# Kernel optimization log

Hardware: AMD Instinct MI355X
Metric: run time of the kernel (lower is better)

Reference implementation:

```python
import jax, jax.numpy as jnp
import numpy as np

D_MODEL = 1024
N_HEADS = 16
D_HEAD = D_MODEL // N_HEADS
D_FF = 4096
B, T = 2, 2048


def layer_norm(x, gamma, beta, eps=1e-5):
    mu = jnp.mean(x, axis=-1, keepdims=True)
    var = jnp.var(x, axis=-1, keepdims=True)
    return (x - mu) * jax.lax.rsqrt(var + eps) * gamma + beta


def setup_inputs() -> dict:
    key = jax.random.key(0)
    ks = jax.random.split(key, 8)
    s = D_MODEL ** -0.5
    return {
        "x": jax.random.normal(ks[0], (B, T, D_MODEL), dtype=jnp.float32),
        "w_qkv": jax.random.normal(ks[1], (D_MODEL, 3 * D_MODEL), dtype=jnp.float32) * s,
        "w_out": jax.random.normal(ks[2], (D_MODEL, D_MODEL), dtype=jnp.float32) * s,
        "ln1_g": jnp.ones((D_MODEL,), jnp.float32),
        "ln1_b": jnp.zeros((D_MODEL,), jnp.float32),
        "ln2_g": jnp.ones((D_MODEL,), jnp.float32),
        "ln2_b": jnp.zeros((D_MODEL,), jnp.float32),
        "w1": jax.random.normal(ks[3], (D_MODEL, D_FF), dtype=jnp.float32) * s,
        "b1": jnp.zeros((D_FF,), jnp.float32),
        "w2": jax.random.normal(ks[4], (D_FF, D_MODEL), dtype=jnp.float32) * (D_FF ** -0.5),
        "b2": jnp.zeros((D_MODEL,), jnp.float32),
    }


def reference(x, w_qkv, w_out, ln1_g, ln1_b, ln2_g, ln2_b, w1, b1, w2, b2):
    Bb, Tt, C = x.shape
    h = layer_norm(x, ln1_g, ln1_b)
    qkv = h @ w_qkv  # [B,T,3C]
    q, k, v = jnp.split(qkv, 3, axis=-1)

    def heads(t):  # [B,T,C] -> [B,H,T,Dh]
        return t.reshape(Bb, Tt, N_HEADS, D_HEAD).transpose(0, 2, 1, 3)

    q, k, v = heads(q), heads(k), heads(v)
    scale = D_HEAD ** -0.5
    attn = jnp.einsum("bhqd,bhkd->bhqk", q, k) * scale
    causal = jnp.tril(jnp.ones((Tt, Tt), dtype=bool))
    attn = jnp.where(causal[None, None], attn, -jnp.inf)
    attn = jax.nn.softmax(attn, axis=-1)
    out = jnp.einsum("bhqk,bhkd->bhqd", attn, v)
    out = out.transpose(0, 2, 1, 3).reshape(Bb, Tt, C)
    x = x + out @ w_out
    h2 = layer_norm(x, ln2_g, ln2_b)
    ff = jax.nn.gelu(h2 @ w1 + b1, approximate=False) @ w2 + b2
    return x + ff
```

## Files before the change

kernel.cpp:

```cpp
#include <hip/hip_runtime.h>
#include <hip/hip_bf16.h>
#include <cstdint>

#define DM 1024
#define DFF 4096
#define NB 2
#define TT 2048
#define NH 16
#define DH 64

typedef unsigned short u16;
typedef __bf16 bf16x8 __attribute__((ext_vector_type(8)));
typedef float f32x4 __attribute__((ext_vector_type(4)));

__device__ __forceinline__ u16 f2b(float f) {
    union { float f; unsigned u; } v; v.f = f;
    unsigned u = v.u;
    return (u16)((u + 0x7FFFu + ((u >> 16) & 1u)) >> 16);
}

__device__ __forceinline__ unsigned cvtpk(float a, float b) {
    unsigned r;
    asm("v_cvt_pk_bf16_f32 %0, %1, %2" : "=v"(r) : "v"(a), "v"(b));
    return r;
}

__device__ __forceinline__ float gelu_fast(float z) {
    const float u = z * z;
    const float w = z * __builtin_fmaf(u, 0.10294324f, 2.3022082f);
    const float e = exp2f(w);
    const float r = __builtin_amdgcn_rcpf(1.0f + e);
    return z - z * r;
}

__device__ __forceinline__ f32x4 mfma_bf16(bf16x8 a, bf16x8 b, f32x4 c) {
    return __builtin_amdgcn_mfma_f32_16x16x32_bf16(a, b, c, 0, 0, 0);
}

__device__ __forceinline__ void gload_lds16(const void* g, void* l) {
    __builtin_amdgcn_global_load_lds((const __attribute__((address_space(1))) unsigned int*)g,
                                     (__attribute__((address_space(3))) unsigned int*)l, 16, 0, 0);
}

__global__ __launch_bounds__(256) void transW(const float* __restrict__ W, u16* __restrict__ Wt,
                                              int K, int N) {
    __shared__ float t[32][33];
    int tx = threadIdx.x & 31, ty = threadIdx.x >> 5;
    int k0 = blockIdx.y * 32, n0 = blockIdx.x * 32;
#pragma unroll
    for (int j = 0; j < 4; ++j)
        t[ty + 8 * j][tx] = W[(size_t)(k0 + ty + 8 * j) * N + n0 + tx];
    __syncthreads();
#pragma unroll
    for (int j = 0; j < 4; ++j)
        Wt[(size_t)(n0 + ty + 8 * j) * K + k0 + tx] = f2b(t[tx][ty + 8 * j]);
}

__global__ __launch_bounds__(256) void ln_kernel(const float* __restrict__ X,
                                                 const float* __restrict__ g,
                                                 const float* __restrict__ bt,
                                                 u16* __restrict__ H) {
    int row = blockIdx.x, tid = threadIdx.x;
    float4 v = ((const float4*)(X + (size_t)row * DM))[tid];
    float s = v.x + v.y + v.z + v.w;
    float ss = v.x * v.x + v.y * v.y + v.z * v.z + v.w * v.w;
#pragma unroll
    for (int off = 32; off >= 1; off >>= 1) {
        s += __shfl_xor(s, off);
        ss += __shfl_xor(ss, off);
    }
    __shared__ float sb[8];
    int w = tid >> 6, lane = tid & 63;
    if (lane == 0) { sb[w] = s; sb[4 + w] = ss; }
    __syncthreads();
    s = sb[0] + sb[1] + sb[2] + sb[3];
    ss = sb[4] + sb[5] + sb[6] + sb[7];
    float mu = s * (1.0f / DM);
    float var = ss * (1.0f / DM) - mu * mu;
    float rstd = rsqrtf(var + 1e-5f);
    float4 gv = ((const float4*)g)[tid];
    float4 bv = ((const float4*)bt)[tid];
    uint2 hv;
    hv.x = cvtpk((v.x - mu) * rstd * gv.x + bv.x, (v.y - mu) * rstd * gv.y + bv.y);
    hv.y = cvtpk((v.z - mu) * rstd * gv.z + bv.z, (v.w - mu) * rstd * gv.w + bv.w);
    ((uint2*)(H + (size_t)row * DM))[tid] = hv;
}

template <int MODE, int DBUF>
__global__ __launch_bounds__(256) void gemm_kernel(
    const u16* __restrict__ A, const u16* __restrict__ Bt, int M, int N, int K,
    u16* __restrict__ oq, u16* __restrict__ ok, u16* __restrict__ vt,
    const float* __restrict__ resid, float* __restrict__ outf,
    const float* __restrict__ bias, u16* __restrict__ outbf) {
    __shared__ __align__(16) u16 Alds[DBUF + 1][128][64];
    __shared__ __align__(16) u16 Blds[DBUF + 1][128][64];
    const int tid = threadIdx.x;
    const int lane = tid & 63;
    const int w = tid >> 6;
    const int wr = w >> 1, wc = w & 1;
    int bid = blockIdx.x + gridDim.x * blockIdx.y;
    const int nwg = gridDim.x * gridDim.y;
    bid = (bid & 7) * (nwg >> 3) + (bid >> 3);
    const int bm = (bid / gridDim.x) * 128, bn = (bid % gridDim.x) * 128;
    const int l15 = lane & 15, lg = lane >> 4;
    const int srow = tid >> 3, pch = tid & 7;
    const int lc = pch ^ (srow & 7);

    f32x4 acc[4][4] = {};
    const u16* Ap = A + (size_t)(bm + srow) * K + lc * 8;
    const u16* Bp = Bt + (size_t)(bn + srow) * K + lc * 8;

#define STAGE(buf, k0)                                                          \
    {                                                                           \
        _Pragma("unroll") for (int i = 0; i < 4; ++i) {                         \
            gload_lds16(Ap + (size_t)(32 * i) * K + (k0), &Alds[buf][srow + 32 * i][pch * 8]); \
            gload_lds16(Bp + (size_t)(32 * i) * K + (k0), &Blds[buf][srow + 32 * i][pch * 8]); \
        }                                                                       \
    }

#define COMPUTE(buf)                                                            \
    {                                                                           \
        _Pragma("unroll") for (int kk = 0; kk < 2; ++kk) {                      \
            bf16x8 af[4], bfr[4];                                               \
            _Pragma("unroll") for (int f = 0; f < 4; ++f) {                     \
                const int ar = wr * 64 + f * 16 + l15;                          \
                const int br = wc * 64 + f * 16 + l15;                          \
                const int kch = kk * 4 + lg;                                    \
                af[f] = *(const bf16x8*)&Alds[buf][ar][(kch ^ (ar & 7)) * 8];   \
                bfr[f] = *(const bf16x8*)&Blds[buf][br][(kch ^ (br & 7)) * 8];  \
            }                                                                   \
            _Pragma("unroll") for (int mi = 0; mi < 4; ++mi)                    \
                _Pragma("unroll") for (int ni = 0; ni < 4; ++ni)                \
                    acc[mi][ni] = mfma_bf16(af[mi], bfr[ni], acc[mi][ni]);      \
        }                                                                       \
    }

    if constexpr (DBUF == 0) {
        for (int k0 = 0; k0 < K; k0 += 64) {
            STAGE(0, k0);
            __syncthreads();
            COMPUTE(0);
            __syncthreads();
        }
    } else {
        STAGE(0, 0);
        for (int k0 = 0; k0 < K; k0 += 64) {
            const int cur = (k0 >> 6) & 1;
            if (k0 + 64 < K) {
                STAGE(cur ^ 1, k0 + 64);
                asm volatile("s_waitcnt vmcnt(8)" ::: "memory");
            } else {
                asm volatile("s_waitcnt vmcnt(0)" ::: "memory");
            }
            __builtin_amdgcn_sched_barrier(0);
            __builtin_amdgcn_s_barrier();
            __builtin_amdgcn_sched_barrier(0);
            COMPUTE(cur);
            __builtin_amdgcn_s_barrier();
        }
    }
#undef STAGE
#undef COMPUTE

    const int m0 = bm + wr * 64, n0 = bn + wc * 64;
#pragma unroll
    for (int mi = 0; mi < 4; ++mi) {
#pragma unroll
        for (int ni = 0; ni < 4; ++ni) {
            if constexpr (MODE == 0) {
                const int n = n0 + ni * 16 + l15;
                const int which = n >> 10;
                const int hh = (n >> 6) & 15, d = n & 63;
                const int mbase = m0 + mi * 16 + 4 * lg;
                const int bb = mbase >> 11, t = mbase & 2047;
                if (which == 2) {
                    uint2 pv;
                    pv.x = cvtpk(acc[mi][ni][0], acc[mi][ni][1]);
                    pv.y = cvtpk(acc[mi][ni][2], acc[mi][ni][3]);
                    *(uint2*)(vt + (((size_t)(bb * NH + hh)) * DH + d) * TT + t) = pv;
                } else {
                    u16* dst = which == 0 ? oq : ok;
                    const float sc = which == 0 ? 0.18033688f : 1.0f;
                    const unsigned p01 = cvtpk(acc[mi][ni][0] * sc, acc[mi][ni][1] * sc);
                    const unsigned p23 = cvtpk(acc[mi][ni][2] * sc, acc[mi][ni][3] * sc);
                    u16* db = dst + (((size_t)(bb * NH + hh)) * TT + t) * DH + d;
                    db[0] = (u16)p01;
                    db[DH] = (u16)(p01 >> 16);
                    db[2 * DH] = (u16)p23;
                    db[3 * DH] = (u16)(p23 >> 16);
                }
            } else if constexpr (MODE == 2) {
                const int n = n0 + ni * 16 + l15;
                const float bn_ = bias[n];
                const float g0 = gelu_fast(acc[mi][ni][0] + bn_);
                const float g1 = gelu_fast(acc[mi][ni][1] + bn_);
                const float g2 = gelu_fast(acc[mi][ni][2] + bn_);
                const float g3 = gelu_fast(acc[mi][ni][3] + bn_);
                const unsigned p01 = cvtpk(g0, g1);
                const unsigned p23 = cvtpk(g2, g3);
                u16* db = outbf + (size_t)(m0 + mi * 16 + 4 * lg) * N + n;
                db[0] = (u16)p01;
                db[N] = (u16)(p01 >> 16);
                db[2 * N] = (u16)p23;
                db[3 * N] = (u16)(p23 >> 16);
            } else {
#pragma unroll
                for (int r = 0; r < 4; ++r) {
                    int m = m0 + mi * 16 + 4 * lg + r;
                    int n = n0 + ni * 16 + l15;
                    float v = acc[mi][ni][r];
                    size_t o = (size_t)m * N + n;
                    if constexpr (MODE == 1) {
                        outf[o] = resid[o] + v;
                    } else {
                        outf[o] = resid[o] + v + bias[n];
                    }
                }
            }
        }
    }
}

__global__ __launch_bounds__(256) void attn_kernel(const u16* __restrict__ Q,
                                                   const u16* __restrict__ Kg,
                                                   const u16* __restrict__ Vtg,
                                                   u16* __restrict__ O) {
    __shared__ __align__(16) u16 Klds[2][64][64];
    __shared__ __align__(16) u16 Vlds[2][64][64];
    const int tid = threadIdx.x, lane = tid & 63, w = tid >> 6;
    const int l15 = lane & 15, lg = lane >> 4;

    int id = blockIdx.x + (blockIdx.y << 4);
    int sw = (id & 7) * 64 + (id >> 3);
    const int p = sw & 15, bh = sw >> 4;
    const size_t base = (size_t)bh * TT * DH;
    const int b = bh >> 4, hh = bh & 15;

    const int srow = tid >> 3, pch = tid & 7;
    const int lc = pch ^ (srow & 7);

    const int src0 = (((2 * lg) & 3) << 4) | l15;
    const int src1 = src0 + 16;
    const bool hi = (lg >> 1) != 0;

#define ASTAGE(buf, kv)                                                                     \
    {                                                                                       \
        gload_lds16(Kg + base + (size_t)((kv) * 64 + srow) * DH + lc * 8,                   \
                    &Klds[buf][srow][pch * 8]);                                             \
        gload_lds16(Kg + base + (size_t)((kv) * 64 + srow + 32) * DH + lc * 8,              \
                    &Klds[buf][srow + 32][pch * 8]);                                        \
        gload_lds16(Vtg + base + (size_t)srow * TT + (kv) * 64 + lc * 8,                    \
                    &Vlds[buf][srow][pch * 8]);                                             \
        gload_lds16(Vtg + base + (size_t)(srow + 32) * TT + (kv) * 64 + lc * 8,             \
                    &Vlds[buf][srow + 32][pch * 8]);                                        \
    }

    for (int half = 0; half < 2; ++half) {
        const int qt = half ? (31 - p) : p;
        const int nkv = qt + 1;
        const int qrow = qt * 64 + w * 16 + l15;
        uint4 qu0 = *(const uint4*)(Q + base + (size_t)qrow * DH + 8 * lg);
        uint4 qu1 = *(const uint4*)(Q + base + (size_t)qrow * DH + 32 + 8 * lg);
        asm volatile("" : "+v"(qu0.x), "+v"(qu0.y), "+v"(qu0.z), "+v"(qu0.w),
                          "+v"(qu1.x), "+v"(qu1.y), "+v"(qu1.z), "+v"(qu1.w));
        const bf16x8 qf0 = *(const bf16x8*)&qu0;
        const bf16x8 qf1 = *(const bf16x8*)&qu1;

        ASTAGE(0, 0);

        f32x4 o[4] = {};
        float mrun = -INFINITY, lsum = 0.0f;

        int cur = 0;
        for (int kv = 0; kv < nkv; ++kv) {
            if (kv + 1 < nkv) {
                ASTAGE(cur ^ 1, kv + 1);
                asm volatile("s_waitcnt vmcnt(4)" ::: "memory");
            } else {
                asm volatile("s_waitcnt vmcnt(0)" ::: "memory");
            }
            __builtin_amdgcn_sched_barrier(0);
            __builtin_amdgcn_s_barrier();
            __builtin_amdgcn_sched_barrier(0);

            f32x4 s[4] = {};
            __builtin_amdgcn_s_setprio(1);
#pragma unroll
            for (int nf = 0; nf < 4; ++nf) {
                const int row = nf * 16 + l15;
                bf16x8 kb0 = *(const bf16x8*)&Klds[cur][row][(lg ^ (l15 & 7)) * 8];
                bf16x8 kb1 = *(const bf16x8*)&Klds[cur][row][((4 + lg) ^ (l15 & 7)) * 8];
                s[nf] = mfma_bf16(kb0, qf0, s[nf]);
                s[nf] = mfma_bf16(kb1, qf1, s[nf]);
            }
            __builtin_amdgcn_s_setprio(0);

            if (kv == qt) {
#pragma unroll
                for (int nf = 0; nf < 4; ++nf) {
                    const int tg = kv * 64 + nf * 16 + 4 * lg;
#pragma unroll
                    for (int r = 0; r < 4; ++r)
                        if (tg + r > qrow) s[nf][r] = -1e30f;
                }
            }

            f32x4 m4 = s[0];
#pragma unroll
            for (int nf = 1; nf < 4; ++nf) {
                m4[0] = fmaxf(m4[0], s[nf][0]);
                m4[1] = fmaxf(m4[1], s[nf][1]);
                m4[2] = fmaxf(m4[2], s[nf][2]);
                m4[3] = fmaxf(m4[3], s[nf][3]);
            }
            float pmax = fmaxf(fmaxf(m4[0], m4[1]), fmaxf(m4[2], m4[3]));
            pmax = fmaxf(pmax, __shfl_xor(pmax, 16));
            pmax = fmaxf(pmax, __shfl_xor(pmax, 32));
            const float mnew = fmaxf(mrun, pmax);
            const float alpha = exp2f(mrun - mnew);
            mrun = mnew;
            float ps = 0.0f;
#pragma unroll
            for (int nf = 0; nf < 4; ++nf) {
#pragma unroll
                for (int r = 0; r < 4; ++r) {
                    const float pp = exp2f(s[nf][r] - mnew);
                    s[nf][r] = pp;
                    ps += pp;
                }
                o[nf] = o[nf] * alpha;
            }
            lsum = lsum * alpha + ps;

            unsigned pk[4][2];
#pragma unroll
            for (int nf = 0; nf < 4; ++nf) {
                pk[nf][0] = cvtpk(s[nf][0], s[nf][1]);
                pk[nf][1] = cvtpk(s[nf][2], s[nf][3]);
            }
            bf16x8 pa[2];
#pragma unroll
            for (int kf = 0; kf < 2; ++kf) {
                unsigned a0 = __shfl((int)pk[2 * kf][0], src0);
                unsigned a1 = __shfl((int)pk[2 * kf][1], src0);
                unsigned a2 = __shfl((int)pk[2 * kf][0], src1);
                unsigned a3 = __shfl((int)pk[2 * kf][1], src1);
                unsigned c0 = __shfl((int)pk[2 * kf + 1][0], src0);
                unsigned c1 = __shfl((int)pk[2 * kf + 1][1], src0);
                unsigned c2 = __shfl((int)pk[2 * kf + 1][0], src1);
                unsigned c3 = __shfl((int)pk[2 * kf + 1][1], src1);
                uint4 wv;
                wv.x = hi ? c0 : a0;
                wv.y = hi ? c1 : a1;
                wv.z = hi ? c2 : a2;
                wv.w = hi ? c3 : a3;
                pa[kf] = *(const bf16x8*)&wv;
            }

            __builtin_amdgcn_s_setprio(1);
#pragma unroll
            for (int nf = 0; nf < 4; ++nf) {
                const int row = nf * 16 + l15;
                bf16x8 vb0 = *(const bf16x8*)&Vlds[cur][row][(lg ^ (l15 & 7)) * 8];
                bf16x8 vb1 = *(const bf16x8*)&Vlds[cur][row][((4 + lg) ^ (l15 & 7)) * 8];
                o[nf] = mfma_bf16(vb0, pa[0], o[nf]);
                o[nf] = mfma_bf16(vb1, pa[1], o[nf]);
            }
            __builtin_amdgcn_s_setprio(0);

            __builtin_amdgcn_s_barrier();
            cur ^= 1;
        }

        lsum += __shfl_xor(lsum, 16);
        lsum += __shfl_xor(lsum, 32);
        const float linv = 1.0f / lsum;
#pragma unroll
        for (int nf = 0; nf < 4; ++nf) {
            uint2 pv;
            pv.x = cvtpk(o[nf][0] * linv, o[nf][1] * linv);
            pv.y = cvtpk(o[nf][2] * linv, o[nf][3] * linv);
            *(uint2*)(O + ((size_t)b * TT + qrow) * DM + hh * DH + nf * 16 + 4 * lg) = pv;
        }
    }
#undef ASTAGE
}

extern "C" void kernel_launch(void* const* d_in, const int* in_sizes, int n_in,
                              void* d_out, int out_size, void* d_ws, size_t ws_size,
                              hipStream_t stream) {
    const float* x = (const float*)d_in[0];
    const float* wqkv = (const float*)d_in[1];
    const float* wout = (const float*)d_in[2];
    const float* ln1g = (const float*)d_in[3];
    const float* ln1b = (const float*)d_in[4];
    const float* ln2g = (const float*)d_in[5];
    const float* ln2b = (const float*)d_in[6];
    const float* w1 = (const float*)d_in[7];
    const float* b1 = (const float*)d_in[8];
    const float* w2 = (const float*)d_in[9];
    const float* b2 = (const float*)d_in[10];
    float* out = (float*)d_out;
    char* ws = (char*)d_ws;

    u16* wqkv_t = (u16*)(ws + 0);
    u16* wout_t = (u16*)(ws + 6291456);
    u16* w1_t   = (u16*)(ws + 8388608);
    u16* w2_t   = (u16*)(ws + 16777216);
    u16* h_bf   = (u16*)(ws + 25165824);
    u16* q_bf   = (u16*)(ws + 33554432);
    u16* k_bf   = (u16*)(ws + 41943040);
    u16* vt_bf  = (u16*)(ws + 50331648);
    u16* at_bf  = (u16*)(ws + 58720256);
    float* x1   = (float*)(ws + 67108864);
    u16* ff1_bf = q_bf;

    transW<<<dim3(96, 32), 256, 0, stream>>>(wqkv, wqkv_t, 1024, 3072);
    transW<<<dim3(32, 32), 256, 0, stream>>>(wout, wout_t, 1024, 1024);
    transW<<<dim3(128, 32), 256, 0, stream>>>(w1, w1_t, 1024, 4096);
    transW<<<dim3(32, 128), 256, 0, stream>>>(w2, w2_t, 4096, 1024);

    ln_kernel<<<4096, 256, 0, stream>>>(x, ln1g, ln1b, h_bf);

    gemm_kernel<0, 1><<<dim3(24, 32), 256, 0, stream>>>(h_bf, wqkv_t, 4096, 3072, 1024,
                                                        q_bf, k_bf, vt_bf,
                                                        nullptr, nullptr, nullptr, nullptr);

    attn_kernel<<<dim3(16, 32), 256, 0, stream>>>(q_bf, k_bf, vt_bf, at_bf);

    gemm_kernel<1, 1><<<dim3(8, 32), 256, 0, stream>>>(at_bf, wout_t, 4096, 1024, 1024,
                                                       nullptr, nullptr, nullptr,
                                                       x, x1, nullptr, nullptr);

    ln_kernel<<<4096, 256, 0, stream>>>(x1, ln2g, ln2b, h_bf);

    gemm_kernel<2, 1><<<dim3(32, 32), 256, 0, stream>>>(h_bf, w1_t, 4096, 4096, 1024,
                                                        nullptr, nullptr, nullptr,
                                                        nullptr, nullptr, b1, ff1_bf);

    gemm_kernel<3, 1><<<dim3(8, 32), 256, 0, stream>>>(ff1_bf, w2_t, 4096, 1024, 4096,
                                                       nullptr, nullptr, nullptr,
                                                       x1, out, b2, nullptr);
}
```

Before: 262.7 us.

## Split-K the FFN down-projection GEMM and add lazy softmax rescaling in attention

The final w2 GEMM (K=4096) now launches twice as many workgroups, each covering half of K. The second half writes raw partial sums into a workspace buffer that a new elementwise add kernel folds into the output. This targets low occupancy: the original grid had only 256 tiles for a long K loop. Attention also skips the running-max update and the rescale of the accumulator and sum unless some lane's new max exceeds the old one by more than 8 (in log2 units). That trades a wavefront vote for fewer multiplies, at the cost of an extra launch and 32MB of extra memory traffic for the partial buffer.

```diff
diff --git a/kernel.cpp b/kernel.cpp
--- a/kernel.cpp
+++ b/kernel.cpp
@@ -86,12 +86,25 @@
     ((uint2*)(H + (size_t)row * DM))[tid] = hv;
 }
 
-template <int MODE, int DBUF>
+__global__ __launch_bounds__(256) void add_kernel(float* __restrict__ out,
+                                                  const float* __restrict__ part, int n4) {
+    int idx = blockIdx.x * 256 + threadIdx.x;
+    const int stride = gridDim.x * 256;
+    for (; idx < n4; idx += stride) {
+        float4 a = ((const float4*)out)[idx];
+        float4 p = ((const float4*)part)[idx];
+        a.x += p.x; a.y += p.y; a.z += p.z; a.w += p.w;
+        ((float4*)out)[idx] = a;
+    }
+}
+
+template <int MODE, int DBUF, int SPLIT>
 __global__ __launch_bounds__(256) void gemm_kernel(
     const u16* __restrict__ A, const u16* __restrict__ Bt, int M, int N, int K,
     u16* __restrict__ oq, u16* __restrict__ ok, u16* __restrict__ vt,
     const float* __restrict__ resid, float* __restrict__ outf,
-    const float* __restrict__ bias, u16* __restrict__ outbf) {
+    const float* __restrict__ bias, u16* __restrict__ outbf,
+    float* __restrict__ part) {
     __shared__ __align__(16) u16 Alds[DBUF + 1][128][64];
     __shared__ __align__(16) u16 Blds[DBUF + 1][128][64];
     const int tid = threadIdx.x;
@@ -101,7 +114,16 @@
     int bid = blockIdx.x + gridDim.x * blockIdx.y;
     const int nwg = gridDim.x * gridDim.y;
     bid = (bid & 7) * (nwg >> 3) + (bid >> 3);
-    const int bm = (bid / gridDim.x) * 128, bn = (bid % gridDim.x) * 128;
+    int mrow = bid / gridDim.x;
+    int ks = 0;
+    if constexpr (SPLIT) {
+        const int mtiles = (nwg / gridDim.x) >> 1;
+        ks = mrow >= mtiles;
+        mrow -= ks * mtiles;
+    }
+    const int bm = mrow * 128, bn = (bid % gridDim.x) * 128;
+    const int kbeg = SPLIT ? ks * (K >> 1) : 0;
+    const int kend = SPLIT ? kbeg + (K >> 1) : K;
     const int l15 = lane & 15, lg = lane >> 4;
     const int srow = tid >> 3, pch = tid & 7;
     const int lc = pch ^ (srow & 7);
@@ -136,17 +158,17 @@
     }
 
     if constexpr (DBUF == 0) {
-        for (int k0 = 0; k0 < K; k0 += 64) {
+        for (int k0 = kbeg; k0 < kend; k0 += 64) {
             STAGE(0, k0);
             __syncthreads();
             COMPUTE(0);
             __syncthreads();
         }
     } else {
-        STAGE(0, 0);
-        for (int k0 = 0; k0 < K; k0 += 64) {
-            const int cur = (k0 >> 6) & 1;
-            if (k0 + 64 < K) {
+        STAGE(0, kbeg);
+        for (int k0 = kbeg; k0 < kend; k0 += 64) {
+            const int cur = ((k0 - kbeg) >> 6) & 1;
+            if (k0 + 64 < kend) {
                 STAGE(cur ^ 1, k0 + 64);
                 asm volatile("s_waitcnt vmcnt(8)" ::: "memory");
             } else {
@@ -213,7 +235,10 @@
                     if constexpr (MODE == 1) {
                         outf[o] = resid[o] + v;
                     } else {
-                        outf[o] = resid[o] + v + bias[n];
+                        if (SPLIT && ks == 1)
+                            part[o] = v;
+                        else
+                            outf[o] = resid[o] + v + bias[n];
                     }
                 }
             }
@@ -316,21 +341,25 @@
             float pmax = fmaxf(fmaxf(m4[0], m4[1]), fmaxf(m4[2], m4[3]));
             pmax = fmaxf(pmax, __shfl_xor(pmax, 16));
             pmax = fmaxf(pmax, __shfl_xor(pmax, 32));
-            const float mnew = fmaxf(mrun, pmax);
-            const float alpha = exp2f(mrun - mnew);
-            mrun = mnew;
+            if (!__all(pmax <= mrun + 8.0f)) {
+                const float mnew = fmaxf(mrun, pmax);
+                const float alpha = exp2f(mrun - mnew);
+                mrun = mnew;
+#pragma unroll
+                for (int nf = 0; nf < 4; ++nf) o[nf] = o[nf] * alpha;
+                lsum *= alpha;
+            }
             float ps = 0.0f;
 #pragma unroll
             for (int nf = 0; nf < 4; ++nf) {
 #pragma unroll
                 for (int r = 0; r < 4; ++r) {
-                    const float pp = exp2f(s[nf][r] - mnew);
+                    const float pp = exp2f(s[nf][r] - mrun);
                     s[nf][r] = pp;
                     ps += pp;
                 }
-                o[nf] = o[nf] * alpha;
-            }
-            lsum = lsum * alpha + ps;
+            }
+            lsum += ps;
 
             unsigned pk[4][2];
 #pragma unroll
@@ -414,6 +443,7 @@
     u16* at_bf  = (u16*)(ws + 58720256);
     float* x1   = (float*)(ws + 67108864);
     u16* ff1_bf = q_bf;
+    float* p1   = (float*)(ws + 0);
 
     transW<<<dim3(96, 32), 256, 0, stream>>>(wqkv, wqkv_t, 1024, 3072);
     transW<<<dim3(32, 32), 256, 0, stream>>>(wout, wout_t, 1024, 1024);
@@ -422,23 +452,27 @@
 
     ln_kernel<<<4096, 256, 0, stream>>>(x, ln1g, ln1b, h_bf);
 
-    gemm_kernel<0, 1><<<dim3(24, 32), 256, 0, stream>>>(h_bf, wqkv_t, 4096, 3072, 1024,
-                                                        q_bf, k_bf, vt_bf,
-                                                        nullptr, nullptr, nullptr, nullptr);
+    gemm_kernel<0, 1, 0><<<dim3(24, 32), 256, 0, stream>>>(h_bf, wqkv_t, 4096, 3072, 1024,
+                                                           q_bf, k_bf, vt_bf,
+                                                           nullptr, nullptr, nullptr, nullptr,
+                                                           nullptr);
 
     attn_kernel<<<dim3(16, 32), 256, 0, stream>>>(q_bf, k_bf, vt_bf, at_bf);
 
-    gemm_kernel<1, 1><<<dim3(8, 32), 256, 0, stream>>>(at_bf, wout_t, 4096, 1024, 1024,
-                                                       nullptr, nullptr, nullptr,
-                                                       x, x1, nullptr, nullptr);
+    gemm_kernel<1, 1, 0><<<dim3(8, 32), 256, 0, stream>>>(at_bf, wout_t, 4096, 1024, 1024,
+                                                          nullptr, nullptr, nullptr,
+                                                          x, x1, nullptr, nullptr, nullptr);
 
     ln_kernel<<<4096, 256, 0, stream>>>(x1, ln2g, ln2b, h_bf);
 
-    gemm_kernel<2, 1><<<dim3(32, 32), 256, 0, stream>>>(h_bf, w1_t, 4096, 4096, 1024,
-                                                        nullptr, nullptr, nullptr,
-                                                        nullptr, nullptr, b1, ff1_bf);
-
-    gemm_kernel<3, 1><<<dim3(8, 32), 256, 0, stream>>>(ff1_bf, w2_t, 4096, 1024, 4096,
-                                                       nullptr, nullptr, nullptr,
-                                                       x1, out, b2, nullptr);
-}
+    gemm_kernel<2, 1, 0><<<dim3(32, 32), 256, 0, stream>>>(h_bf, w1_t, 4096, 4096, 1024,
+                                                           nullptr, nullptr, nullptr,
+                                                           nullptr, nullptr, b1, ff1_bf,
+                                                           nullptr);
+
+    gemm_kernel<3, 1, 1><<<dim3(8, 64), 256, 0, stream>>>(ff1_bf, w2_t, 4096, 1024, 4096,
+                                                          nullptr, nullptr, nullptr,
+                                                          x1, out, b2, nullptr, p1);
+
+    add_kernel<<<2048, 256, 0, stream>>>(out, p1, 4096 * 1024 / 4);
+}
```

Result: faster. 254.0 us (-3.3%).
